# Kernel tuning notes

Measured on AMD Instinct MI355X. Metric: run time of the kernel, lower is better.

Reference implementation:

```python
import jax, jax.numpy as jnp
import numpy as np

DIM = 1024
HIDDEN = 3072
SCALE = 1.0 / 127.0  # fixed Q8_0-style dequant scale from QuantizedLinear


def setup_inputs() -> dict:
    key = jax.random.key(0)
    k_x, k_g, k_u, k_d = jax.random.split(key, 4)
    x = jax.random.normal(k_x, (4, 2048, DIM), dtype=jnp.float32)
    # int8-valued quantized weights stored as int32 (symmetric range like torch int8 weights)
    w_gate = jax.random.randint(k_g, (HIDDEN, DIM), -127, 128, dtype=jnp.int32)
    w_up = jax.random.randint(k_u, (HIDDEN, DIM), -127, 128, dtype=jnp.int32)
    w_down = jax.random.randint(k_d, (DIM, HIDDEN), -127, 128, dtype=jnp.int32)
    return {"x": x, "w_gate": w_gate, "w_up": w_up, "w_down": w_down}


def _dequant(w_int, dtype):
    return w_int.astype(dtype) * jnp.asarray(SCALE, dtype)


def reference(x, w_gate, w_up, w_down):
    # QuantizedLinear: dequantize int8 weight to x.dtype, then F.linear (x @ W^T)
    wg = _dequant(w_gate, x.dtype)   # [H, D]
    wu = _dequant(w_up, x.dtype)     # [H, D]
    wd = _dequant(w_down, x.dtype)   # [D, H]
    gate = jnp.einsum('bsd,hd->bsh', x, wg)
    up = jnp.einsum('bsd,hd->bsh', x, wu)
    h = jax.nn.silu(gate) * up       # SwiGLU elementwise fusion
    return jnp.einsum('bsh,dh->bsd', h, wd)
```

## Files before the change

### kernel.cpp

```cpp
#include <hip/hip_runtime.h>
#include <hip/hip_bf16.h>


typedef __attribute__((ext_vector_type(8))) __bf16 bf16x8;
typedef __attribute__((ext_vector_type(4))) float f32x4;

static constexpr float QS = 1.0f / 127.0f;

#define BAR()    asm volatile("s_barrier" ::: "memory")
#define VMCNT4() asm volatile("s_waitcnt vmcnt(4)" ::: "memory")
#define VMCNT0() asm volatile("s_waitcnt vmcnt(0)" ::: "memory")
#define LGKM8()  asm volatile("s_waitcnt lgkmcnt(8)" ::: "memory")
#define PRIO1()  __builtin_amdgcn_s_setprio(1)
#define PRIO0()  __builtin_amdgcn_s_setprio(0)
#define SB0()    __builtin_amdgcn_sched_barrier(0)

__device__ __forceinline__ void gload_lds16(const void* g, void* l) {
  __builtin_amdgcn_global_load_lds(
      (const __attribute__((address_space(1))) void*)g,
      (__attribute__((address_space(3))) void*)l,
      16, 0, 0);
}


__global__ __launch_bounds__(256) void k_conv_x(const float* __restrict__ x,
                                                __bf16* __restrict__ xb, int n8) {
  int t = blockIdx.x * 256 + threadIdx.x;
  if (t >= n8) return;
  const float4* p = (const float4*)(x + (size_t)t * 8);
  float4 a = p[0], b = p[1];
  bf16x8 o;
  o[0] = (__bf16)a.x; o[1] = (__bf16)a.y; o[2] = (__bf16)a.z; o[3] = (__bf16)a.w;
  o[4] = (__bf16)b.x; o[5] = (__bf16)b.y; o[6] = (__bf16)b.z; o[7] = (__bf16)b.w;
  *(bf16x8*)(xb + (size_t)t * 8) = o;
}

__global__ __launch_bounds__(256) void k_conv_w1(const int* __restrict__ wg,
                                                 const int* __restrict__ wu,
                                                 __bf16* __restrict__ w1) {
  int t = blockIdx.x * 256 + threadIdx.x;
  int c8 = t & 127;
  int v = t >> 7;
  int bb = v >> 5, tt = v & 31;
  const int* src = (tt < 16) ? (wg + (size_t)(bb * 16 + tt) * 1024)
                             : (wu + (size_t)(bb * 16 + (tt & 15)) * 1024);
  const int4* p = (const int4*)(src + c8 * 8);
  int4 a = p[0], b = p[1];
  bf16x8 o;
  o[0] = (__bf16)(float)a.x; o[1] = (__bf16)(float)a.y;
  o[2] = (__bf16)(float)a.z; o[3] = (__bf16)(float)a.w;
  o[4] = (__bf16)(float)b.x; o[5] = (__bf16)(float)b.y;
  o[6] = (__bf16)(float)b.z; o[7] = (__bf16)(float)b.w;
  *(bf16x8*)(w1 + (size_t)v * 1024 + c8 * 8) = o;
}

__global__ __launch_bounds__(256) void k_conv_wd(const int* __restrict__ wdn,
                                                 __bf16* __restrict__ wdb, int n8) {
  int t = blockIdx.x * 256 + threadIdx.x;
  if (t >= n8) return;
  const int4* p = (const int4*)(wdn + (size_t)t * 8);
  int4 a = p[0], b = p[1];
  bf16x8 o;
  o[0] = (__bf16)(float)a.x; o[1] = (__bf16)(float)a.y;
  o[2] = (__bf16)(float)a.z; o[3] = (__bf16)(float)a.w;
  o[4] = (__bf16)(float)b.x; o[5] = (__bf16)(float)b.y;
  o[6] = (__bf16)(float)b.z; o[7] = (__bf16)(float)b.w;
  *(bf16x8*)(wdb + (size_t)t * 8) = o;
}


#define MFMA16(MG, NG)                                                         \
  _Pragma("unroll") for (int mi = 0; mi < 4; ++mi) {                           \
    _Pragma("unroll") for (int nj = 0; nj < 2; ++nj) {                         \
      acc[(MG)*4 + mi][(NG)*2 + nj] = __builtin_amdgcn_mfma_f32_16x16x32_bf16( \
          af[mi][0], bf[NG][nj][0], acc[(MG)*4 + mi][(NG)*2 + nj], 0, 0, 0);   \
      acc[(MG)*4 + mi][(NG)*2 + nj] = __builtin_amdgcn_mfma_f32_16x16x32_bf16( \
          af[mi][1], bf[NG][nj][1], acc[(MG)*4 + mi][(NG)*2 + nj], 0, 0, 0);   \
    }                                                                          \
  }

#define LDAF(MG)                                                               \
  _Pragma("unroll") for (int mi = 0; mi < 4; ++mi) {                           \
    af[mi][0] = *(const bf16x8*)(aL + ((MG)*64 + mi * 16 + r16) * 128 + s0);   \
    af[mi][1] = *(const bf16x8*)(aL + ((MG)*64 + mi * 16 + r16) * 128 + s1);   \
  }

#define LDBF(NG)                                                               \
  _Pragma("unroll") for (int nj = 0; nj < 2; ++nj) {                           \
    bf[NG][nj][0] = *(const bf16x8*)(bL + (bro + (NG)*32 + nj * 16) * 128 + s0); \
    bf[NG][nj][1] = *(const bf16x8*)(bL + (bro + (NG)*32 + nj * 16) * 128 + s1); \
  }

__global__ __launch_bounds__(512, 2) void k_gemm1_8p(const __bf16* __restrict__ A,
                                                     const __bf16* __restrict__ Bp,
                                                     __bf16* __restrict__ Out) {
  constexpr int LDAK = 1024, NT = 16, LDO = 3072;
  const int row0 = blockIdx.y * 256, col0 = blockIdx.x * 256;
  const int kz = 0;
  __shared__ __bf16 sA[2][2][128][64];
  __shared__ __bf16 sB[2][2][128][64];
  const int tid = threadIdx.x;
  const int lane = tid & 63;
  const int wid = tid >> 6;
  const int wm = wid >> 2, wn = wid & 3;
  const int r16 = lane & 15;
  const int kq = lane >> 4;

  auto STG = [&](__bf16* dst, const __bf16* src, int rbase, int kt) {
    int r0 = tid >> 3;
    int c0 = (tid & 7) ^ (r0 & 7);
    int r1 = 64 + r0;
    gload_lds16(src + (size_t)(rbase + r0) * LDAK + kt * 64 + c0 * 8,
                dst + tid * 8);
    gload_lds16(src + (size_t)(rbase + r1) * LDAK + kt * 64 + c0 * 8,
                dst + (512 + tid) * 8);
  };

  f32x4 acc[8][4] = {};

  STG(&sA[0][0][0][0], A, row0, kz);
  STG(&sB[0][0][0][0], Bp, col0, kz);
  STG(&sA[0][1][0][0], A, row0 + 128, kz);
  STG(&sB[0][1][0][0], Bp, col0 + 128, kz);
  const int kt1 = kz + 1;
  STG(&sB[1][0][0][0], Bp, col0, kt1);
  STG(&sA[1][0][0][0], A, row0, kt1);
  VMCNT4();
  BAR();

  for (int t = 0; t < NT; ++t) {
    const int c = t & 1;
    const char* aL = (const char*)&sA[c][wm][0][0];
    const char* bL = (const char*)&sB[c][wn >> 1][0][0];
    const int bro = (wn & 1) * 64 + r16;
    const int s0 = ((kq) ^ (r16 & 7)) << 4;
    const int s1 = ((4 + kq) ^ (r16 & 7)) << 4;
    const int k1 = kz + (t + 1 < NT ? t + 1 : NT - 1);
    const int k2 = kz + (t + 2 < NT ? t + 2 : NT - 1);
    bf16x8 af[4][2], bf[2][2][2];

    LDAF(0);
    LDBF(0);
    LGKM8();
    STG(&sA[c ^ 1][1][0][0], A, row0 + 128, k1);
    BAR();
    PRIO1(); MFMA16(0, 0); PRIO0();
    BAR();
    LDBF(1);
    STG(&sB[c ^ 1][1][0][0], Bp, col0 + 128, k1);
    BAR();
    PRIO1(); MFMA16(0, 1); PRIO0();
    BAR();
    LDAF(1);
    STG(&sB[c][0][0][0], Bp, col0, k2);
    BAR();
    PRIO1(); MFMA16(1, 0); PRIO0();
    BAR();
    STG(&sA[c][0][0][0], A, row0, k2);
    BAR();
    PRIO1(); MFMA16(1, 1); PRIO0();
    VMCNT4();
    BAR();
  }

  __bf16* hout = Out;
  const int hbase = (col0 + wn * 64) >> 1;
#pragma unroll
  for (int i = 0; i < 8; ++i) {
#pragma unroll
    for (int p = 0; p < 2; ++p) {
#pragma unroll
      for (int rr = 0; rr < 4; ++rr) {
        int row = row0 + wm * 128 + i * 16 + kq * 4 + rr;
        float g = acc[i][2 * p][rr] * QS;
        float u = acc[i][2 * p + 1][rr] * QS;
        float hv = (g / (1.0f + __expf(-g))) * u;
        hout[(size_t)row * LDO + hbase + p * 16 + r16] = (__bf16)hv;
      }
    }
  }
  VMCNT0();
}

__global__ __launch_bounds__(256) void k_gemm2a(const __bf16* __restrict__ H,
                                                const __bf16* __restrict__ Bw,
                                                float* __restrict__ out) {
  __shared__ __bf16 sA[128][64];
  __shared__ __bf16 sB[128][64];
  const int b = blockIdx.x;
  const int xcd = b & 7, ii = b >> 3;
  const int z = ii >> 6;
  const int rem = ii & 63;
  const int yy = rem >> 3, xx = rem & 7;
  const int row0 = (xcd * 8 + yy) * 128, col0 = xx * 128;
  const int kz = z * 24;

  const int tid = threadIdx.x;
  const int lane = tid & 63;
  const int wid = tid >> 6;
  const int wm = wid >> 1, wn = wid & 1;
  const int r16 = lane & 15;
  const int kq = lane >> 4;

  f32x4 acc[4][4] = {};

  for (int kt = kz; kt < kz + 24; ++kt) {
    __syncthreads();
#pragma unroll
    for (int it = 0; it < 4; ++it) {
      int chunk = it * 256 + tid;
      int r = chunk >> 3, kc = chunk & 7;
      int kcs = kc ^ (r & 7);
      gload_lds16(H + (size_t)(row0 + r) * 3072 + kt * 64 + kcs * 8,
                  ((__bf16*)sA) + chunk * 8);
      gload_lds16(Bw + (size_t)(col0 + r) * 3072 + kt * 64 + kcs * 8,
                  ((__bf16*)sB) + chunk * 8);
    }
    __syncthreads();
#pragma unroll
    for (int ks = 0; ks < 2; ++ks) {
      const int chs = ((ks * 4 + kq) ^ (r16 & 7)) << 4;
      bf16x8 av[4], bv[4];
#pragma unroll
      for (int i = 0; i < 4; ++i)
        av[i] = *(const bf16x8*)(((const char*)sA) +
                                 (wm * 64 + i * 16 + r16) * 128 + chs);
#pragma unroll
      for (int j = 0; j < 4; ++j)
        bv[j] = *(const bf16x8*)(((const char*)sB) +
                                 (wn * 64 + j * 16 + r16) * 128 + chs);
#pragma unroll
      for (int i = 0; i < 4; ++i)
#pragma unroll
        for (int j = 0; j < 4; ++j)
          acc[i][j] = __builtin_amdgcn_mfma_f32_16x16x32_bf16(av[i], bv[j],
                                                              acc[i][j], 0, 0, 0);
    }
  }

#pragma unroll
  for (int i = 0; i < 4; ++i)
#pragma unroll
    for (int j = 0; j < 4; ++j)
#pragma unroll
      for (int r = 0; r < 4; ++r) {
        int row = row0 + wm * 64 + i * 16 + kq * 4 + r;
        int col = col0 + wn * 64 + j * 16 + r16;
        atomicAdd(out + (size_t)row * 1024 + col, acc[i][j][r] * QS);
      }
}


extern "C" void kernel_launch(void* const* d_in, const int* in_sizes, int n_in,
                              void* d_out, int out_size, void* d_ws, size_t ws_size,
                              hipStream_t stream) {
  const float* x = (const float*)d_in[0];
  const int* wg = (const int*)d_in[1];
  const int* wu = (const int*)d_in[2];
  const int* wd = (const int*)d_in[3];

  char* ws = (char*)d_ws;
  __bf16* xb  = (__bf16*)(ws);
  __bf16* w1  = (__bf16*)(ws + 16777216);
  __bf16* wdb = (__bf16*)(ws + 16777216 + 12582912);
  __bf16* h   = (__bf16*)(ws + 35651584);

  hipMemsetAsync(d_out, 0, (size_t)8192 * 1024 * sizeof(float), stream);

  k_conv_x<<<4096, 256, 0, stream>>>(x, xb, 1048576);
  k_conv_w1<<<3072, 256, 0, stream>>>(wg, wu, w1);
  k_conv_wd<<<1536, 256, 0, stream>>>(wd, wdb, 393216);

  k_gemm1_8p<<<dim3(24, 32), 512, 0, stream>>>(xb, w1, h);
  k_gemm2a<<<1024, 256, 0, stream>>>(h, wdb, (float*)d_out);
}
```

Before: 327.5 us.

## Merge conversion kernels and drop split-K atomics in down projection

Three separate conversion launches (x to bf16, gate/up weights, down weights) become one kernel that dispatches on block index, saving launch overhead. The down-projection GEMM no longer splits K in two with atomicAdd into a zeroed output. Each block now covers the full K range of 48 tiles and stores its result directly, which also removes the memset. The trade-off is half as many blocks (512) for the second GEMM, so there is less parallelism to fill the GPU.

```diff
diff --git a/kernel.cpp b/kernel.cpp
--- a/kernel.cpp
+++ b/kernel.cpp
@@ -13,7 +13,6 @@
 #define LGKM8()  asm volatile("s_waitcnt lgkmcnt(8)" ::: "memory")
 #define PRIO1()  __builtin_amdgcn_s_setprio(1)
 #define PRIO0()  __builtin_amdgcn_s_setprio(0)
-#define SB0()    __builtin_amdgcn_sched_barrier(0)
 
 __device__ __forceinline__ void gload_lds16(const void* g, void* l) {
   __builtin_amdgcn_global_load_lds(
@@ -22,50 +21,48 @@
       16, 0, 0);
 }
 
-
-__global__ __launch_bounds__(256) void k_conv_x(const float* __restrict__ x,
-                                                __bf16* __restrict__ xb, int n8) {
-  int t = blockIdx.x * 256 + threadIdx.x;
-  if (t >= n8) return;
-  const float4* p = (const float4*)(x + (size_t)t * 8);
-  float4 a = p[0], b = p[1];
-  bf16x8 o;
-  o[0] = (__bf16)a.x; o[1] = (__bf16)a.y; o[2] = (__bf16)a.z; o[3] = (__bf16)a.w;
-  o[4] = (__bf16)b.x; o[5] = (__bf16)b.y; o[6] = (__bf16)b.z; o[7] = (__bf16)b.w;
-  *(bf16x8*)(xb + (size_t)t * 8) = o;
-}
-
-__global__ __launch_bounds__(256) void k_conv_w1(const int* __restrict__ wg,
-                                                 const int* __restrict__ wu,
-                                                 __bf16* __restrict__ w1) {
-  int t = blockIdx.x * 256 + threadIdx.x;
-  int c8 = t & 127;
-  int v = t >> 7;
-  int bb = v >> 5, tt = v & 31;
-  const int* src = (tt < 16) ? (wg + (size_t)(bb * 16 + tt) * 1024)
-                             : (wu + (size_t)(bb * 16 + (tt & 15)) * 1024);
-  const int4* p = (const int4*)(src + c8 * 8);
-  int4 a = p[0], b = p[1];
-  bf16x8 o;
-  o[0] = (__bf16)(float)a.x; o[1] = (__bf16)(float)a.y;
-  o[2] = (__bf16)(float)a.z; o[3] = (__bf16)(float)a.w;
-  o[4] = (__bf16)(float)b.x; o[5] = (__bf16)(float)b.y;
-  o[6] = (__bf16)(float)b.z; o[7] = (__bf16)(float)b.w;
-  *(bf16x8*)(w1 + (size_t)v * 1024 + c8 * 8) = o;
-}
-
-__global__ __launch_bounds__(256) void k_conv_wd(const int* __restrict__ wdn,
-                                                 __bf16* __restrict__ wdb, int n8) {
-  int t = blockIdx.x * 256 + threadIdx.x;
-  if (t >= n8) return;
-  const int4* p = (const int4*)(wdn + (size_t)t * 8);
-  int4 a = p[0], b = p[1];
-  bf16x8 o;
-  o[0] = (__bf16)(float)a.x; o[1] = (__bf16)(float)a.y;
-  o[2] = (__bf16)(float)a.z; o[3] = (__bf16)(float)a.w;
-  o[4] = (__bf16)(float)b.x; o[5] = (__bf16)(float)b.y;
-  o[6] = (__bf16)(float)b.z; o[7] = (__bf16)(float)b.w;
-  *(bf16x8*)(wdb + (size_t)t * 8) = o;
+__global__ __launch_bounds__(256) void k_conv_all(const float* __restrict__ x,
+                                                  __bf16* __restrict__ xb,
+                                                  const int* __restrict__ wg,
+                                                  const int* __restrict__ wu,
+                                                  __bf16* __restrict__ w1,
+                                                  const int* __restrict__ wdn,
+                                                  __bf16* __restrict__ wdb) {
+  int b = blockIdx.x;
+  if (b < 4096) {
+    int t = b * 256 + threadIdx.x;
+    const float4* p = (const float4*)(x + (size_t)t * 8);
+    float4 a = p[0], c = p[1];
+    bf16x8 o;
+    o[0] = (__bf16)a.x; o[1] = (__bf16)a.y; o[2] = (__bf16)a.z; o[3] = (__bf16)a.w;
+    o[4] = (__bf16)c.x; o[5] = (__bf16)c.y; o[6] = (__bf16)c.z; o[7] = (__bf16)c.w;
+    *(bf16x8*)(xb + (size_t)t * 8) = o;
+  } else if (b < 7168) {
+    int t = (b - 4096) * 256 + threadIdx.x;
+    int c8 = t & 127;
+    int v = t >> 7;
+    int bb = v >> 5, tt = v & 31;
+    const int* src = (tt < 16) ? (wg + (size_t)(bb * 16 + tt) * 1024)
+                               : (wu + (size_t)(bb * 16 + (tt & 15)) * 1024);
+    const int4* p = (const int4*)(src + c8 * 8);
+    int4 a = p[0], c = p[1];
+    bf16x8 o;
+    o[0] = (__bf16)(float)a.x; o[1] = (__bf16)(float)a.y;
+    o[2] = (__bf16)(float)a.z; o[3] = (__bf16)(float)a.w;
+    o[4] = (__bf16)(float)c.x; o[5] = (__bf16)(float)c.y;
+    o[6] = (__bf16)(float)c.z; o[7] = (__bf16)(float)c.w;
+    *(bf16x8*)(w1 + (size_t)v * 1024 + c8 * 8) = o;
+  } else {
+    int t = (b - 7168) * 256 + threadIdx.x;
+    const int4* p = (const int4*)(wdn + (size_t)t * 8);
+    int4 a = p[0], c = p[1];
+    bf16x8 o;
+    o[0] = (__bf16)(float)a.x; o[1] = (__bf16)(float)a.y;
+    o[2] = (__bf16)(float)a.z; o[3] = (__bf16)(float)a.w;
+    o[4] = (__bf16)(float)c.x; o[5] = (__bf16)(float)c.y;
+    o[6] = (__bf16)(float)c.z; o[7] = (__bf16)(float)c.w;
+    *(bf16x8*)(wdb + (size_t)t * 8) = o;
+  }
 }
 
 
@@ -182,18 +179,16 @@
   VMCNT0();
 }
 
-__global__ __launch_bounds__(256) void k_gemm2a(const __bf16* __restrict__ H,
+__global__ __launch_bounds__(256) void k_gemm2b(const __bf16* __restrict__ H,
                                                 const __bf16* __restrict__ Bw,
                                                 float* __restrict__ out) {
   __shared__ __bf16 sA[128][64];
   __shared__ __bf16 sB[128][64];
   const int b = blockIdx.x;
   const int xcd = b & 7, ii = b >> 3;
-  const int z = ii >> 6;
-  const int rem = ii & 63;
-  const int yy = rem >> 3, xx = rem & 7;
-  const int row0 = (xcd * 8 + yy) * 128, col0 = xx * 128;
-  const int kz = z * 24;
+  const int yl = ii >> 2, xl = ii & 3;
+  const int row0 = ((xcd & 3) * 16 + yl) * 128;
+  const int col0 = ((xcd >> 2) * 4 + xl) * 128;
 
   const int tid = threadIdx.x;
   const int lane = tid & 63;
@@ -204,7 +199,7 @@
 
   f32x4 acc[4][4] = {};
 
-  for (int kt = kz; kt < kz + 24; ++kt) {
+  for (int kt = 0; kt < 48; ++kt) {
     __syncthreads();
 #pragma unroll
     for (int it = 0; it < 4; ++it) {
@@ -246,7 +241,7 @@
       for (int r = 0; r < 4; ++r) {
         int row = row0 + wm * 64 + i * 16 + kq * 4 + r;
         int col = col0 + wn * 64 + j * 16 + r16;
-        atomicAdd(out + (size_t)row * 1024 + col, acc[i][j][r] * QS);
+        out[(size_t)row * 1024 + col] = acc[i][j][r] * QS;
       }
 }
 
@@ -265,12 +260,7 @@
   __bf16* wdb = (__bf16*)(ws + 16777216 + 12582912);
   __bf16* h   = (__bf16*)(ws + 35651584);
 
-  hipMemsetAsync(d_out, 0, (size_t)8192 * 1024 * sizeof(float), stream);
-
-  k_conv_x<<<4096, 256, 0, stream>>>(x, xb, 1048576);
-  k_conv_w1<<<3072, 256, 0, stream>>>(wg, wu, w1);
-  k_conv_wd<<<1536, 256, 0, stream>>>(wd, wdb, 393216);
-
+  k_conv_all<<<8704, 256, 0, stream>>>(x, xb, wg, wu, w1, wd, wdb);
   k_gemm1_8p<<<dim3(24, 32), 512, 0, stream>>>(xb, w1, h);
-  k_gemm2a<<<1024, 256, 0, stream>>>(h, wdb, (float*)d_out);
-}
+  k_gemm2b<<<512, 256, 0, stream>>>(h, wdb, (float*)d_out);
+}
```

Result: faster. 274.2 us (-16.3%).
